# Optimization experiments

Hardware: AMD Instinct MI355X
Metric: run time of the kernel (lower is better)

The kernel has to match this reference:

```python
import jax, jax.numpy as jnp
import numpy as np

B, T, I, H, L, O = 32, 512, 256, 512, 2, 128

def setup_inputs() -> dict:
    key = jax.random.key(0)
    ks = jax.random.split(key, 11)
    s_i = 1.0 / np.sqrt(H)
    inp = {"x": jax.random.normal(ks[0], (B, T, I), jnp.float32)}
    for l in range(L):
        in_dim = I if l == 0 else H
        inp[f"W_ih_{l}"] = jax.random.uniform(ks[1 + 4 * l], (3 * H, in_dim), jnp.float32, -s_i, s_i)
        inp[f"W_hh_{l}"] = jax.random.uniform(ks[2 + 4 * l], (3 * H, H), jnp.float32, -s_i, s_i)
        inp[f"b_ih_{l}"] = jax.random.uniform(ks[3 + 4 * l], (3 * H,), jnp.float32, -s_i, s_i)
        inp[f"b_hh_{l}"] = jax.random.uniform(ks[4 + 4 * l], (3 * H,), jnp.float32, -s_i, s_i)
    inp["fc_W"] = jax.random.uniform(ks[9], (O, H), jnp.float32, -s_i, s_i)
    inp["fc_b"] = jax.random.uniform(ks[10], (O,), jnp.float32, -s_i, s_i)
    return inp

def _gru_layer(x, W_ih, W_hh, b_ih, b_hh):
    # x: [B,T,in] -> precompute input projections once (big batched GEMM)
    xp = jnp.einsum('bti,gi->btg', x, W_ih) + b_ih  # [B,T,3H]
    h0 = jnp.zeros((x.shape[0], W_hh.shape[1]), x.dtype)
    def step(h, xt):  # xt: [B,3H]
        gh = h @ W_hh.T + b_hh  # [B,3H]
        xr, xz, xn = jnp.split(xt, 3, axis=-1)
        hr, hz, hn = jnp.split(gh, 3, axis=-1)
        r = jax.nn.sigmoid(xr + hr)
        z = jax.nn.sigmoid(xz + hz)
        n = jnp.tanh(xn + r * hn)
        h_new = (1.0 - z) * n + z * h
        return h_new, h_new
    hT, ys = jax.lax.scan(step, h0, jnp.swapaxes(xp, 0, 1))  # ys: [T,B,H]
    return jnp.swapaxes(ys, 0, 1), hT

def reference(x, W_ih_0, W_hh_0, b_ih_0, b_hh_0, W_ih_1, W_hh_1, b_ih_1, b_hh_1, fc_W, fc_b):
    layers = [(W_ih_0, W_hh_0, b_ih_0, b_hh_0), (W_ih_1, W_hh_1, b_ih_1, b_hh_1)]
    h = x
    finals = []
    for (Wi, Wh, bi, bh) in layers:
        h, hT = _gru_layer(h, Wi, Wh, bi, bh)
        finals.append(hT)
    hidden = jnp.stack(finals, axis=0)  # [L,B,H]
    out = jnp.einsum('bth,oh->bto', h, fc_W) + fc_b  # [B,T,O]
    return out, hidden
```

## Files before the change

### kernel.cpp

```cpp
#include <hip/hip_runtime.h>
#include <math.h>

#define Bsz 32
#define Tt  512
#define Isz 256
#define Hsz 512
#define G3  1536
#define Osz 128

#define NBLK 256
#define TPB  512
#define G0_L0 1u
#define G0_L1 4096u
#define POLL_GUARD (1 << 22)

typedef float f4  __attribute__((ext_vector_type(4)));
typedef unsigned int u32;
typedef u32 u32x2 __attribute__((ext_vector_type(2)));

__device__ __forceinline__ float sigf(float x) { return 1.0f / (1.0f + expf(-x)); }

__global__ void init_pbuf(u32x2* pbuf, u32 gen0) {
    int i = threadIdx.x + blockIdx.x * blockDim.x;
    const int n = Bsz * Hsz;
    for (; i < n; i += gridDim.x * blockDim.x) {
        pbuf[i]     = (u32x2){0u, gen0};
        pbuf[n + i] = (u32x2){0u, 0u};
    }
}

__global__ void __launch_bounds__(TPB)
__attribute__((amdgpu_waves_per_eu(2, 2)))
gru_rec(
    const float* __restrict__ xp,
    const float* __restrict__ Whh,
    const float* __restrict__ bhh,
    float* __restrict__ hall,
    u32x2* __restrict__ pbuf,
    float* __restrict__ hid_out,
    u32 g0)
{
    const int tid = threadIdx.x;
    const int b   = blockIdx.x & 31;
    const int p   = blockIdx.x >> 5;
    const int jl  = tid >> 3;
    const int kc  = tid & 7;
    const int j   = p * 64 + jl;

    __shared__ float hsh[8 * 68];

    f4 wreg[3][16];
    #pragma unroll
    for (int g = 0; g < 3; ++g) {
        const float* wp = Whh + (size_t)(g * Hsz + j) * Hsz + kc * 64;
        #pragma unroll
        for (int q = 0; q < 16; ++q)
            wreg[g][q] = *reinterpret_cast<const f4*>(wp + q * 4);
    }
    #pragma unroll
    for (int g = 0; g < 3; ++g)
        #pragma unroll
        for (int q = 0; q < 16; ++q)
            asm volatile("" : "+v"(wreg[g][q]));

    const float bh0 = bhh[0 * Hsz + j];
    const float bh1 = bhh[1 * Hsz + j];
    const float bh2 = bhh[2 * Hsz + j];

    for (int t = 0; t < Tt; ++t) {
        const u32 rg = g0 + (u32)t;
        const u32 wg = rg + 1u;
        const u32x2* src = pbuf + (size_t)(t & 1) * (Bsz * Hsz) + b * Hsz;
        u32x2*       dst = pbuf + (size_t)((t + 1) & 1) * (Bsz * Hsz) + b * Hsz;

        float xr = 0.f, xz = 0.f, xn = 0.f;
        if (kc == 0) {
            const float* pp = xp + (size_t)(b * Tt + t) * G3;
            xr = pp[j];
            xz = pp[Hsz + j];
            xn = pp[2 * Hsz + j];
        }

        {
            const u32x2* sp = src + tid;
            int guard = 0;
            for (;;) {
                u32x2 pr;
                asm volatile("global_load_dwordx2 %0, %1, off sc0 sc1\n\t"
                             "s_waitcnt vmcnt(0)"
                             : "=&v"(pr) : "v"(sp) : "memory");
                if (__all(pr[1] == rg) || ++guard > POLL_GUARD) {
                    hsh[(tid >> 6) * 68 + (tid & 63)] = __uint_as_float(pr[0]);
                    break;
                }
                __builtin_amdgcn_s_sleep(1);
            }
        }
        __syncthreads();

        float a0 = 0.f, a1 = 0.f, a2 = 0.f;
        {
            const f4* hp = reinterpret_cast<const f4*>(hsh) + kc * 17;
            #pragma unroll
            for (int q = 0; q < 16; ++q) {
                f4 hv4 = hp[q];
                a0 = fmaf(wreg[0][q][0], hv4[0], a0);
                a0 = fmaf(wreg[0][q][1], hv4[1], a0);
                a0 = fmaf(wreg[0][q][2], hv4[2], a0);
                a0 = fmaf(wreg[0][q][3], hv4[3], a0);
                a1 = fmaf(wreg[1][q][0], hv4[0], a1);
                a1 = fmaf(wreg[1][q][1], hv4[1], a1);
                a1 = fmaf(wreg[1][q][2], hv4[2], a1);
                a1 = fmaf(wreg[1][q][3], hv4[3], a1);
                a2 = fmaf(wreg[2][q][0], hv4[0], a2);
                a2 = fmaf(wreg[2][q][1], hv4[1], a2);
                a2 = fmaf(wreg[2][q][2], hv4[2], a2);
                a2 = fmaf(wreg[2][q][3], hv4[3], a2);
            }
        }

        #pragma unroll
        for (int off = 1; off < 8; off <<= 1) {
            a0 += __shfl_xor(a0, off, 64);
            a1 += __shfl_xor(a1, off, 64);
            a2 += __shfl_xor(a2, off, 64);
        }

        if (kc == 0) {
            float rr = sigf(xr + a0 + bh0);
            float zz = sigf(xz + a1 + bh1);
            float nn = tanhf(xn + rr * (a2 + bh2));
            float ho = hsh[(j >> 6) * 68 + (j & 63)];
            float hv = (1.0f - zz) * nn + zz * ho;
            u32x2 pk = (u32x2){__float_as_uint(hv), wg};
            asm volatile("global_store_dwordx2 %0, %1, off sc0 sc1"
                         :: "v"(dst + j), "v"(pk) : "memory");
            hall[(size_t)(b * Tt + t) * Hsz + j] = hv;
            if (t == Tt - 1) hid_out[b * Hsz + j] = hv;
        }

        __syncthreads();
    }
}

#define GM 64
#define GN 64
#define GK 16
__global__ void __launch_bounds__(256) gemm_nt_bias(
    const float* __restrict__ A, const float* __restrict__ W,
    const float* __restrict__ bias, float* __restrict__ C,
    int M, int N, int K)
{
    __shared__ float As[GK][GM];
    __shared__ float Bs[GK][GN];
    const int tid = threadIdx.x;
    const int n0 = blockIdx.x * GN;
    const int m0 = blockIdx.y * GM;
    const int tn = tid & 15;
    const int tm = tid >> 4;
    const int lrow = tid >> 2;
    const int lkq  = tid & 3;

    float acc[4][4];
    #pragma unroll
    for (int i = 0; i < 4; ++i)
        #pragma unroll
        for (int jj = 0; jj < 4; ++jj) acc[i][jj] = 0.0f;

    for (int k0 = 0; k0 < K; k0 += GK) {
        float4 av = *reinterpret_cast<const float4*>(&A[(size_t)(m0 + lrow) * K + k0 + lkq * 4]);
        float4 wv = *reinterpret_cast<const float4*>(&W[(size_t)(n0 + lrow) * K + k0 + lkq * 4]);
        __syncthreads();
        As[lkq * 4 + 0][lrow] = av.x; As[lkq * 4 + 1][lrow] = av.y;
        As[lkq * 4 + 2][lrow] = av.z; As[lkq * 4 + 3][lrow] = av.w;
        Bs[lkq * 4 + 0][lrow] = wv.x; Bs[lkq * 4 + 1][lrow] = wv.y;
        Bs[lkq * 4 + 2][lrow] = wv.z; Bs[lkq * 4 + 3][lrow] = wv.w;
        __syncthreads();
        #pragma unroll
        for (int k = 0; k < GK; ++k) {
            float4 a4 = *reinterpret_cast<const float4*>(&As[k][tm * 4]);
            float4 b4 = *reinterpret_cast<const float4*>(&Bs[k][tn * 4]);
            acc[0][0] = fmaf(a4.x, b4.x, acc[0][0]); acc[0][1] = fmaf(a4.x, b4.y, acc[0][1]);
            acc[0][2] = fmaf(a4.x, b4.z, acc[0][2]); acc[0][3] = fmaf(a4.x, b4.w, acc[0][3]);
            acc[1][0] = fmaf(a4.y, b4.x, acc[1][0]); acc[1][1] = fmaf(a4.y, b4.y, acc[1][1]);
            acc[1][2] = fmaf(a4.y, b4.z, acc[1][2]); acc[1][3] = fmaf(a4.y, b4.w, acc[1][3]);
            acc[2][0] = fmaf(a4.z, b4.x, acc[2][0]); acc[2][1] = fmaf(a4.z, b4.y, acc[2][1]);
            acc[2][2] = fmaf(a4.z, b4.z, acc[2][2]); acc[2][3] = fmaf(a4.z, b4.w, acc[2][3]);
            acc[3][0] = fmaf(a4.w, b4.x, acc[3][0]); acc[3][1] = fmaf(a4.w, b4.y, acc[3][1]);
            acc[3][2] = fmaf(a4.w, b4.z, acc[3][2]); acc[3][3] = fmaf(a4.w, b4.w, acc[3][3]);
        }
    }

    float4 bb = *reinterpret_cast<const float4*>(&bias[n0 + tn * 4]);
    #pragma unroll
    for (int i = 0; i < 4; ++i) {
        int m = m0 + tm * 4 + i;
        float4 o;
        o.x = acc[i][0] + bb.x; o.y = acc[i][1] + bb.y;
        o.z = acc[i][2] + bb.z; o.w = acc[i][3] + bb.w;
        *reinterpret_cast<float4*>(&C[(size_t)m * N + n0 + tn * 4]) = o;
    }
}

extern "C" void kernel_launch(void* const* d_in, const int* in_sizes, int n_in,
                              void* d_out, int out_size, void* d_ws, size_t ws_size,
                              hipStream_t stream) {
    (void)in_sizes; (void)n_in; (void)out_size; (void)ws_size;
    const float* x    = (const float*)d_in[0];
    const float* Wih0 = (const float*)d_in[1];
    const float* Whh0 = (const float*)d_in[2];
    const float* bih0 = (const float*)d_in[3];
    const float* bhh0 = (const float*)d_in[4];
    const float* Wih1 = (const float*)d_in[5];
    const float* Whh1 = (const float*)d_in[6];
    const float* bih1 = (const float*)d_in[7];
    const float* bhh1 = (const float*)d_in[8];
    const float* fcW  = (const float*)d_in[9];
    const float* fcb  = (const float*)d_in[10];

    float* out = (float*)d_out;
    float* hid = out + (size_t)Bsz * Tt * Osz;

    char* ws = (char*)d_ws;
    const size_t xp_off   = 0;
    const size_t hall_off = xp_off + (size_t)Bsz * Tt * G3 * 4;
    const size_t pbuf_off = hall_off + (size_t)Bsz * Tt * Hsz * 4;
    float* xp    = (float*)(ws + xp_off);
    float* hall  = (float*)(ws + hall_off);
    u32x2* pbuf  = (u32x2*)(ws + pbuf_off);

    hipLaunchKernelGGL(gemm_nt_bias, dim3(G3 / GN, (Bsz * Tt) / GM), dim3(256), 0, stream,
                       x, Wih0, bih0, xp, Bsz * Tt, G3, Isz);

    hipLaunchKernelGGL(init_pbuf, dim3(64), dim3(256), 0, stream, pbuf, G0_L0);
    hipLaunchKernelGGL(gru_rec, dim3(NBLK), dim3(TPB), 0, stream,
                       xp, Whh0, bhh0, hall, pbuf, hid, G0_L0);

    hipLaunchKernelGGL(gemm_nt_bias, dim3(G3 / GN, (Bsz * Tt) / GM), dim3(256), 0, stream,
                       hall, Wih1, bih1, xp, Bsz * Tt, G3, Hsz);

    hipLaunchKernelGGL(init_pbuf, dim3(64), dim3(256), 0, stream, pbuf, G0_L1);
    hipLaunchKernelGGL(gru_rec, dim3(NBLK), dim3(TPB), 0, stream,
                       xp, Whh1, bhh1, hall, pbuf, hid + Bsz * Hsz, G0_L1);

    hipLaunchKernelGGL(gemm_nt_bias, dim3(Osz / GN, (Bsz * Tt) / GM), dim3(256), 0, stream,
                       hall, fcW, fcb, out, Bsz * Tt, Osz, Hsz);
}
```

Measured before the change: 2.322 ms.

## Use fp16 MFMA for input-projection GEMMs and packed FMA in recurrence

Replaces the scalar fp32 tiled GEMM for the two input projections with an MFMA 16x16x32 f16 kernel. Activations are converted to half on the fly and the weights are pre-converted by a new conversion kernel. The recurrent matvec now uses v_pk_fma_f32 on float2 pairs, roughly halving its FMA instruction count. The half-precision inputs risk accuracy loss, and the MFMA kernel reads A and B straight from global memory with no LDS staging.

After: 2.527 ms. 1.09x slower.

```diff
diff --git a/kernel.cpp b/kernel.cpp
--- a/kernel.cpp
+++ b/kernel.cpp
@@ -14,11 +14,27 @@
 #define G0_L1 4096u
 #define POLL_GUARD (1 << 22)
 
+typedef float f2  __attribute__((ext_vector_type(2)));
 typedef float f4  __attribute__((ext_vector_type(4)));
+typedef float f32x4 __attribute__((ext_vector_type(4)));
+typedef _Float16 half8_t __attribute__((ext_vector_type(8)));
+typedef _Float16 half4_t __attribute__((ext_vector_type(4)));
 typedef unsigned int u32;
 typedef u32 u32x2 __attribute__((ext_vector_type(2)));
 
 __device__ __forceinline__ float sigf(float x) { return 1.0f / (1.0f + expf(-x)); }
+
+__global__ void f32_to_f16(const float* __restrict__ in, _Float16* __restrict__ out, int n4) {
+    int i = threadIdx.x + blockIdx.x * blockDim.x;
+    int stride = blockDim.x * gridDim.x;
+    for (int k = i; k < n4; k += stride) {
+        float4 v = reinterpret_cast<const float4*>(in)[k];
+        half4_t o;
+        o[0] = (_Float16)v.x; o[1] = (_Float16)v.y;
+        o[2] = (_Float16)v.z; o[3] = (_Float16)v.w;
+        reinterpret_cast<half4_t*>(out)[k] = o;
+    }
+}
 
 __global__ void init_pbuf(u32x2* pbuf, u32 gen0) {
     int i = threadIdx.x + blockIdx.x * blockDim.x;
@@ -49,19 +65,18 @@
 
     __shared__ float hsh[8 * 68];
 
-    f4 wreg[3][16];
+    f2 wreg2[3][32];
     #pragma unroll
     for (int g = 0; g < 3; ++g) {
-        const float* wp = Whh + (size_t)(g * Hsz + j) * Hsz + kc * 64;
-        #pragma unroll
-        for (int q = 0; q < 16; ++q)
-            wreg[g][q] = *reinterpret_cast<const f4*>(wp + q * 4);
+        const f2* wp2 = reinterpret_cast<const f2*>(Whh + (size_t)(g * Hsz + j) * Hsz + kc * 64);
+        #pragma unroll
+        for (int q = 0; q < 32; ++q) wreg2[g][q] = wp2[q];
     }
     #pragma unroll
     for (int g = 0; g < 3; ++g)
         #pragma unroll
-        for (int q = 0; q < 16; ++q)
-            asm volatile("" : "+v"(wreg[g][q]));
+        for (int q = 0; q < 32; ++q)
+            asm volatile("" : "+v"(wreg2[g][q]));
 
     const float bh0 = bhh[0 * Hsz + j];
     const float bh1 = bhh[1 * Hsz + j];
@@ -98,26 +113,20 @@
         }
         __syncthreads();
 
-        float a0 = 0.f, a1 = 0.f, a2 = 0.f;
+        f2 c0 = (f2){0.f, 0.f}, c1 = (f2){0.f, 0.f}, c2 = (f2){0.f, 0.f};
         {
-            const f4* hp = reinterpret_cast<const f4*>(hsh) + kc * 17;
+            const f2* hp2 = reinterpret_cast<const f2*>(hsh + kc * 68);
             #pragma unroll
-            for (int q = 0; q < 16; ++q) {
-                f4 hv4 = hp[q];
-                a0 = fmaf(wreg[0][q][0], hv4[0], a0);
-                a0 = fmaf(wreg[0][q][1], hv4[1], a0);
-                a0 = fmaf(wreg[0][q][2], hv4[2], a0);
-                a0 = fmaf(wreg[0][q][3], hv4[3], a0);
-                a1 = fmaf(wreg[1][q][0], hv4[0], a1);
-                a1 = fmaf(wreg[1][q][1], hv4[1], a1);
-                a1 = fmaf(wreg[1][q][2], hv4[2], a1);
-                a1 = fmaf(wreg[1][q][3], hv4[3], a1);
-                a2 = fmaf(wreg[2][q][0], hv4[0], a2);
-                a2 = fmaf(wreg[2][q][1], hv4[1], a2);
-                a2 = fmaf(wreg[2][q][2], hv4[2], a2);
-                a2 = fmaf(wreg[2][q][3], hv4[3], a2);
+            for (int q = 0; q < 32; ++q) {
+                f2 hv = hp2[q];
+                asm volatile("v_pk_fma_f32 %0, %1, %2, %0" : "+v"(c0) : "v"(wreg2[0][q]), "v"(hv));
+                asm volatile("v_pk_fma_f32 %0, %1, %2, %0" : "+v"(c1) : "v"(wreg2[1][q]), "v"(hv));
+                asm volatile("v_pk_fma_f32 %0, %1, %2, %0" : "+v"(c2) : "v"(wreg2[2][q]), "v"(hv));
             }
         }
+        float a0 = c0[0] + c0[1];
+        float a1 = c1[0] + c1[1];
+        float a2 = c2[0] + c2[1];
 
         #pragma unroll
         for (int off = 1; off < 8; off <<= 1) {
@@ -140,6 +149,68 @@
         }
 
         __syncthreads();
+    }
+}
+
+__global__ void __launch_bounds__(256) gemm_nt_mfma(
+    const float* __restrict__ A,
+    const _Float16* __restrict__ Wh,
+    const float* __restrict__ bias,
+    float* __restrict__ C,
+    int M, int N, int K)
+{
+    const int tid = threadIdx.x;
+    const int l   = tid & 63;
+    const int w   = tid >> 6;
+    const int wm  = w >> 1, wn = w & 1;
+    const int m0  = blockIdx.y * 128 + wm * 64;
+    const int n0  = blockIdx.x * 128 + wn * 64;
+    const int lr  = l & 15;
+    const int lk  = (l >> 4) * 8;
+
+    f32x4 acc[4][4];
+    #pragma unroll
+    for (int mt = 0; mt < 4; ++mt)
+        #pragma unroll
+        for (int nt = 0; nt < 4; ++nt)
+            acc[mt][nt] = (f32x4){0.f, 0.f, 0.f, 0.f};
+
+    for (int ks = 0; ks < K; ks += 32) {
+        half8_t af[4], bf[4];
+        #pragma unroll
+        for (int mt = 0; mt < 4; ++mt) {
+            const float* pa = A + (size_t)(m0 + mt * 16 + lr) * K + ks + lk;
+            float4 v0 = *reinterpret_cast<const float4*>(pa);
+            float4 v1 = *reinterpret_cast<const float4*>(pa + 4);
+            half8_t h;
+            h[0] = (_Float16)v0.x; h[1] = (_Float16)v0.y;
+            h[2] = (_Float16)v0.z; h[3] = (_Float16)v0.w;
+            h[4] = (_Float16)v1.x; h[5] = (_Float16)v1.y;
+            h[6] = (_Float16)v1.z; h[7] = (_Float16)v1.w;
+            af[mt] = h;
+        }
+        #pragma unroll
+        for (int nt = 0; nt < 4; ++nt)
+            bf[nt] = *reinterpret_cast<const half8_t*>(Wh + (size_t)(n0 + nt * 16 + lr) * K + ks + lk);
+        #pragma unroll
+        for (int mt = 0; mt < 4; ++mt)
+            #pragma unroll
+            for (int nt = 0; nt < 4; ++nt)
+                acc[mt][nt] = __builtin_amdgcn_mfma_f32_16x16x32_f16(af[mt], bf[nt], acc[mt][nt], 0, 0, 0);
+    }
+
+    #pragma unroll
+    for (int nt = 0; nt < 4; ++nt) {
+        const int colg = n0 + nt * 16 + lr;
+        const float bb = bias[colg];
+        #pragma unroll
+        for (int mt = 0; mt < 4; ++mt) {
+            #pragma unroll
+            for (int r = 0; r < 4; ++r) {
+                int rowg = m0 + mt * 16 + (l >> 4) * 4 + r;
+                C[(size_t)rowg * N + colg] = acc[mt][nt][r] + bb;
+            }
+        }
     }
 }
 
@@ -225,19 +296,26 @@
     const size_t xp_off   = 0;
     const size_t hall_off = xp_off + (size_t)Bsz * Tt * G3 * 4;
     const size_t pbuf_off = hall_off + (size_t)Bsz * Tt * Hsz * 4;
-    float* xp    = (float*)(ws + xp_off);
-    float* hall  = (float*)(ws + hall_off);
-    u32x2* pbuf  = (u32x2*)(ws + pbuf_off);
-
-    hipLaunchKernelGGL(gemm_nt_bias, dim3(G3 / GN, (Bsz * Tt) / GM), dim3(256), 0, stream,
-                       x, Wih0, bih0, xp, Bsz * Tt, G3, Isz);
+    const size_t w0h_off  = pbuf_off + (size_t)2 * Bsz * Hsz * 8;
+    const size_t w1h_off  = w0h_off + (size_t)G3 * Isz * 2;
+    float*     xp    = (float*)(ws + xp_off);
+    float*     hall  = (float*)(ws + hall_off);
+    u32x2*     pbuf  = (u32x2*)(ws + pbuf_off);
+    _Float16*  W0h   = (_Float16*)(ws + w0h_off);
+    _Float16*  W1h   = (_Float16*)(ws + w1h_off);
+
+    hipLaunchKernelGGL(f32_to_f16, dim3(128), dim3(256), 0, stream, Wih0, W0h, G3 * Isz / 4);
+    hipLaunchKernelGGL(f32_to_f16, dim3(256), dim3(256), 0, stream, Wih1, W1h, G3 * Hsz / 4);
+
+    hipLaunchKernelGGL(gemm_nt_mfma, dim3(G3 / 128, (Bsz * Tt) / 128), dim3(256), 0, stream,
+                       x, W0h, bih0, xp, Bsz * Tt, G3, Isz);
 
     hipLaunchKernelGGL(init_pbuf, dim3(64), dim3(256), 0, stream, pbuf, G0_L0);
     hipLaunchKernelGGL(gru_rec, dim3(NBLK), dim3(TPB), 0, stream,
                        xp, Whh0, bhh0, hall, pbuf, hid, G0_L0);
 
-    hipLaunchKernelGGL(gemm_nt_bias, dim3(G3 / GN, (Bsz * Tt) / GM), dim3(256), 0, stream,
-                       hall, Wih1, bih1, xp, Bsz * Tt, G3, Hsz);
+    hipLaunchKernelGGL(gemm_nt_mfma, dim3(G3 / 128, (Bsz * Tt) / 128), dim3(256), 0, stream,
+                       hall, W1h, bih1, xp, Bsz * Tt, G3, Hsz);
 
     hipLaunchKernelGGL(init_pbuf, dim3(64), dim3(256), 0, stream, pbuf, G0_L1);
     hipLaunchKernelGGL(gru_rec, dim3(NBLK), dim3(TPB), 0, stream,
```
